# Kernel optimization log

Hardware: AMD Instinct MI355X
Metric: run time of the kernel (lower is better)

The kernel has to match this reference:

```python
import jax, jax.numpy as jnp
import numpy as np

N, C, L, K = 150000, 256, 50000, 200  # nodes, classes(=feature dim), labeled count, top-k


def setup_inputs() -> dict:
    key = jax.random.key(0)
    k1, k2 = jax.random.split(key)
    inputs = jax.random.normal(k1, (N, C), dtype=jnp.float32)
    cls = jax.random.randint(k2, (N,), 0, C)
    labels = jax.nn.one_hot(cls, C, dtype=jnp.float32)  # one-hot label matrix [N, C]
    labels_mask = jnp.arange(N) < L      # first L nodes labeled
    unlabels_mask = ~labels_mask
    return {"inputs": inputs, "labels": labels, "labels_mask": labels_mask,
            "unlabels_mask": unlabels_mask, "k": K}


def _l2n(x):
    # tf.nn.l2_normalize with epsilon 1e-12
    return x * jax.lax.rsqrt(jnp.maximum(jnp.sum(x * x, axis=-1, keepdims=True), 1e-12))


def reference(inputs, labels, labels_mask, unlabels_mask, k):
    lm = labels_mask.astype(inputs.dtype)    # [N]
    um = unlabels_mask.astype(inputs.dtype)  # [N]
    # protos: per-class mean of labeled features (masked matmul == boolean_mask + matmul)
    total = jnp.einsum('nf,nc->fc', inputs * lm[:, None], labels)  # [F, C]
    weight = 1.0 / jnp.sum(labels, 0)                               # 1/count per class (over ALL labels, as in TF)
    protos = (total * weight[None, :]).T                            # [C, F]
    # cosine similarity of every node to every prototype [N, C]
    prob = _l2n(inputs) @ _l2n(protos).T
    # per-row top-k, scattered back to a sparse [N, C] (raw top values, softmax in TF was dead code)
    vals, idx = jax.lax.top_k(prob, k)                              # [N, k]
    rows = jnp.arange(prob.shape[0])[:, None]
    sparse = jnp.zeros_like(prob).at[rows, idx].set(vals)
    p = sparse * um[:, None]                                        # only unlabeled rows contribute
    # per-class normalization: denom_c = sum_u p[u,c] + n_labeled_c
    denom = jnp.sum(p, 0) + jnp.sum(labels * lm[:, None], 0)        # [C]
    w = p / denom[None, :]                                          # [N, C]
    # change[c] = sum_u w[u,c] * (x_u - protos[c])
    change = w.T @ inputs - jnp.sum(w, 0)[:, None] * protos         # [C, F]
    protos = protos + change
    logits = _l2n(inputs) @ _l2n(protos).T                          # [N, C]
    return logits
```

## Files before the change

kernel.cpp:

```cpp
#include <hip/hip_runtime.h>

typedef unsigned int uint;
typedef unsigned short ushort;
typedef float f32x4 __attribute__((ext_vector_type(4)));
typedef uint u32x4 __attribute__((ext_vector_type(4)));
typedef uint u32x2 __attribute__((ext_vector_type(2)));
typedef __bf16 bf16x8 __attribute__((ext_vector_type(8)));

constexpr int NR = 150000;
constexpr int CD = 256;
constexpr int LR = 50000;
constexpr int KEX = 56;
constexpr int NB1 = 49984;
constexpr int NUP = 100032;
constexpr int NTP = 150080;
constexpr int NPB = NTP / 64;
constexpr int NCB = 1024;
constexpr int NFB = NPB + NCB;

__device__ __forceinline__ ushort f2bf(float x) {
  uint u = __builtin_bit_cast(uint, x);
  u += 0x7FFFu + ((u >> 16) & 1u);
  return (ushort)(u >> 16);
}
__device__ __forceinline__ uint key16(uint b) {
  return (b & 0x8000u) ? (~b & 0xFFFFu) : (b | 0x8000u);
}
__device__ __forceinline__ float bfval(uint p) {
  return __builtin_bit_cast(float, p << 16);
}

__global__ __launch_bounds__(256) void k_pre(const float* __restrict__ X,
                                             const float* __restrict__ labels,
                                             ushort* __restrict__ Xt,
                                             float* __restrict__ invn,
                                             int* __restrict__ cls,
                                             float* __restrict__ ca,
                                             float* __restrict__ cl) {
  __shared__ __align__(16) char sm[34816];
  int t = threadIdx.x;
  uint bx = blockIdx.x;
  uint ia = (bx * (uint)NCB) / (uint)NFB;
  uint ib = ((bx + 1) * (uint)NCB) / (uint)NFB;
  if (ib > ia) {
    int* ha = (int*)sm;
    int* hl = (int*)(sm + 1024);
    ha[t] = 0; hl[t] = 0;
    __syncthreads();
    int lane = t & 63;
    int wid = ((int)ia << 2) | (t >> 6);
    int nw = NCB << 2;
    int n = wid;
    for (; n + 3 * nw < NR; n += 4 * nw) {
      f32x4 v[4];
#pragma unroll
      for (int u = 0; u < 4; ++u)
        v[u] = *reinterpret_cast<const f32x4*>(&labels[(size_t)(n + u * nw) * CD + lane * 4]);
#pragma unroll
      for (int u = 0; u < 4; ++u) {
        int nn = n + u * nw;
        int j = v[u][0] > 0.5f ? 0 : v[u][1] > 0.5f ? 1 : v[u][2] > 0.5f ? 2
                                                        : v[u][3] > 0.5f ? 3 : -1;
        if (j >= 0) {
          int c = lane * 4 + j;
          cls[nn] = c;
          atomicAdd(&ha[c], 1);
          if (nn < LR) atomicAdd(&hl[c], 1);
        }
      }
    }
    for (; n < NR; n += nw) {
      f32x4 v = *reinterpret_cast<const f32x4*>(&labels[(size_t)n * CD + lane * 4]);
      int j = v[0] > 0.5f ? 0 : v[1] > 0.5f ? 1 : v[2] > 0.5f ? 2 : v[3] > 0.5f ? 3 : -1;
      if (j >= 0) {
        int c = lane * 4 + j;
        cls[n] = c;
        atomicAdd(&ha[c], 1);
        if (n < LR) atomicAdd(&hl[c], 1);
      }
    }
    __syncthreads();
    atomicAdd(&ca[t], (float)ha[t]);
    atomicAdd(&cl[t], (float)hl[t]);
  } else {
    int pb = (int)(bx - ia);
    ushort* xl = (ushort*)sm;
    float* red = (float*)(sm + 33792);
    int r = t >> 2, cq = t & 3;
    int g0 = pb * 64;
    int g = g0 + r;
    bool valid = g < NR;
    float ss = 0.f;
#pragma unroll
    for (int j = 0; j < 16; ++j) {
      int col = cq * 4 + j * 16;
      f32x4 x = valid ? *reinterpret_cast<const f32x4*>(&X[g * CD + col])
                      : (f32x4){0.f, 0.f, 0.f, 0.f};
      ss += x[0] * x[0] + x[1] * x[1] + x[2] * x[2] + x[3] * x[3];
      uint p0 = (uint)f2bf(x[0]) | ((uint)f2bf(x[1]) << 16);
      uint p1 = (uint)f2bf(x[2]) | ((uint)f2bf(x[3]) << 16);
      *reinterpret_cast<u32x2*>(&xl[r * 264 + col]) = (u32x2){p0, p1};
    }
    red[t] = ss;
    __syncthreads();
    if (t < 64) {
      float s4 = red[t * 4] + red[t * 4 + 1] + red[t * 4 + 2] + red[t * 4 + 3];
      if (g0 + t < NR) invn[g0 + t] = rsqrtf(fmaxf(s4, 1e-12f));
    }
    ushort* xp = Xt + (size_t)pb * 16384;
    int f = t;
    uint buf[4];
    for (int n = 0; n < 64; ++n) {
      ushort v16 = xl[n * 264 + f];
      int sl = n & 7;
      if (sl & 1) buf[sl >> 1] |= (uint)v16 << 16; else buf[sl >> 1] = v16;
      if (sl == 7)
        *reinterpret_cast<u32x4*>(&xp[f * 64 + n - 7]) =
            (u32x4){buf[0], buf[1], buf[2], buf[3]};
    }
  }
}

template <int KIND>
__global__ __launch_bounds__(1024) void k_gemmB(const int* __restrict__ cls,
                                                const ushort* __restrict__ Ap,
                                                const ushort* __restrict__ Xt,
                                                float* __restrict__ P,
                                                int nch, int nbase) {
  __shared__ __align__(16) ushort Al[256 * 40];
  __shared__ __align__(16) ushort Bl[256 * 40];
  int t = threadIdx.x;
  int lane = t & 63, w = t >> 6;
  int m = lane & 15, qd = lane >> 4;
  int cR = t >> 2, off = (t & 3) * 8;
  f32x4 acc[16];
#pragma unroll
  for (int i = 0; i < 16; ++i) acc[i] = (f32x4){0.f, 0.f, 0.f, 0.f};

  if (KIND == 0) {
    for (int i = t; i < 5120; i += 1024) reinterpret_cast<uint*>(Al)[i] = 0u;
  }

  u32x4 aR, bR;
  int curc = -1, prevc = -1;
  int ch = blockIdx.x;
  if (ch < nch) {
    int n0 = ch * 32;
    if (KIND == 1) {
      const ushort* ap = Ap + (size_t)(n0 >> 6) * 16384 + (n0 & 63);
      aR = *reinterpret_cast<const u32x4*>(&ap[cR * 64 + off]);
    } else if (t < 32) {
      int gg = n0 + t;
      curc = (gg < LR) ? cls[gg] : -1;
    }
    int gr = nbase + n0;
    const ushort* xp = Xt + (size_t)(gr >> 6) * 16384 + (gr & 63);
    bR = *reinterpret_cast<const u32x4*>(&xp[cR * 64 + off]);
  }

  for (; ch < nch; ch += gridDim.x) {
    __syncthreads();
    if (KIND == 0) {
      if (t < 32) {
        if (prevc >= 0) Al[prevc * 40 + t] = 0;
        if (curc >= 0) Al[curc * 40 + t] = 0x3F80;
        prevc = curc;
      }
    } else {
      *reinterpret_cast<u32x4*>(&Al[cR * 40 + off]) = aR;
    }
    *reinterpret_cast<u32x4*>(&Bl[cR * 40 + off]) = bR;
    int chn = ch + gridDim.x;
    if (chn < nch) {
      int n0 = chn * 32;
      if (KIND == 1) {
        const ushort* ap = Ap + (size_t)(n0 >> 6) * 16384 + (n0 & 63);
        aR = *reinterpret_cast<const u32x4*>(&ap[cR * 64 + off]);
      } else if (t < 32) {
        int gg = n0 + t;
        curc = (gg < LR) ? cls[gg] : -1;
      }
      int gr = nbase + n0;
      const ushort* xp = Xt + (size_t)(gr >> 6) * 16384 + (gr & 63);
      bR = *reinterpret_cast<const u32x4*>(&xp[cR * 64 + off]);
    }
    __syncthreads();
    bf16x8 a = *reinterpret_cast<const bf16x8*>(&Al[(w * 16 + m) * 40 + qd * 8]);
#pragma unroll
    for (int ft = 0; ft < 16; ++ft) {
      bf16x8 b = *reinterpret_cast<const bf16x8*>(&Bl[(ft * 16 + m) * 40 + qd * 8]);
      acc[ft] = __builtin_amdgcn_mfma_f32_16x16x32_bf16(a, b, acc[ft], 0, 0, 0);
    }
  }
  float* Ps = P + (size_t)blockIdx.x * 65536;
#pragma unroll
  for (int ft = 0; ft < 16; ++ft)
#pragma unroll
    for (int r = 0; r < 4; ++r)
      Ps[(w * 16 + qd * 4 + r) * 256 + ft * 16 + m] = acc[ft][r];
}

__global__ __launch_bounds__(256) void k_protos(const float* __restrict__ P, int nsl,
                                                const float* __restrict__ ca,
                                                float* __restrict__ protos,
                                                ushort* __restrict__ phat) {
  __shared__ float red[256];
  int c = blockIdx.x, f = threadIdx.x;
  float s = 0.f;
  for (int i = 0; i < nsl; ++i) s += P[i * 65536 + c * 256 + f];
  float cnt = ca[c];
  float pv = cnt > 0.5f ? s / cnt : 0.f;
  protos[c * 256 + f] = pv;
  red[f] = pv * pv;
  __syncthreads();
  for (int st = 128; st > 0; st >>= 1) {
    if (f < st) red[f] += red[f + st];
    __syncthreads();
  }
  float iv = rsqrtf(fmaxf(red[0], 1e-12f));
  phat[c * 256 + f] = f2bf(pv * iv);
}

__global__ __launch_bounds__(256) void k_update(const float* __restrict__ PS, int nsl,
                                                const float* __restrict__ protos,
                                                const float* __restrict__ q,
                                                const float* __restrict__ clab,
                                                ushort* __restrict__ phat2) {
  __shared__ float red[256];
  int c = blockIdx.x, f = threadIdx.x;
  float s = 0.f;
  for (int i = 0; i < nsl; ++i) s += PS[i * 65536 + c * 256 + f];
  float qc = q[c];
  float den = qc + clab[c];
  float pv = protos[c * 256 + f];
  float np = pv + (s - qc * pv) / den;
  red[f] = np * np;
  __syncthreads();
  for (int st = 128; st > 0; st >>= 1) {
    if (f < st) red[f] += red[f + st];
    __syncthreads();
  }
  float iv = rsqrtf(fmaxf(red[0], 1e-12f));
  phat2[c * 256 + f] = f2bf(np * iv);
}

template <int TOPK>
__global__ __launch_bounds__(256, 4) void k_passA(const float* __restrict__ X,
                                                  const float* __restrict__ invn,
                                                  const ushort* __restrict__ Bm,
                                                  float* __restrict__ out,
                                                  ushort* __restrict__ pt,
                                                  float* __restrict__ q,
                                                  int gbase) {
  __shared__ __align__(16) char smem[TOPK ? 35840 : 20480];
  ushort* Bl = reinterpret_cast<ushort*>(smem);
  float* qlds = reinterpret_cast<float*>(smem + 34816);
  int t = threadIdx.x;
  int lane = t & 63, w = t >> 6;
  int m = lane & 15, qd = lane >> 4;
  int g0 = gbase + blockIdx.x * 64;
  int g2 = g0 + w * 16 + m;
  bool vA = g2 < NR;
  float inv2 = vA ? invn[g2] : 0.f;
  const float* xp = X + (size_t)(vA ? g2 : 0) * CD + qd * 8;
  int cB = t >> 2, offB = (t & 3) * 8;
  if (TOPK) qlds[t] = 0.f;
  f32x4 acc[16];
#pragma unroll
  for (int i = 0; i < 16; ++i) acc[i] = (f32x4){0.f, 0.f, 0.f, 0.f};

  f32x4 x0 = *reinterpret_cast<const f32x4*>(&xp[0]);
  f32x4 x1 = *reinterpret_cast<const f32x4*>(&xp[4]);
  u32x4 bR[4];
#pragma unroll
  for (int i = 0; i < 4; ++i)
    bR[i] = *reinterpret_cast<const u32x4*>(&Bm[(cB + i * 64) * 256 + offB]);

  for (int k0 = 0; k0 < 256; k0 += 32) {
    f32x4 y0 = x0 * inv2, y1 = x1 * inv2;
    uint u0 = (uint)f2bf(y0[0]) | ((uint)f2bf(y0[1]) << 16);
    uint u1 = (uint)f2bf(y0[2]) | ((uint)f2bf(y0[3]) << 16);
    uint u2 = (uint)f2bf(y1[0]) | ((uint)f2bf(y1[1]) << 16);
    uint u3 = (uint)f2bf(y1[2]) | ((uint)f2bf(y1[3]) << 16);
    u32x4 au = (u32x4){u0, u1, u2, u3};
    bf16x8 a = __builtin_bit_cast(bf16x8, au);
    __syncthreads();
#pragma unroll
    for (int i = 0; i < 4; ++i)
      *reinterpret_cast<u32x4*>(&Bl[(cB + i * 64) * 40 + offB]) = bR[i];
    if (k0 < 224) {
      int kn = k0 + 32;
      x0 = *reinterpret_cast<const f32x4*>(&xp[kn]);
      x1 = *reinterpret_cast<const f32x4*>(&xp[kn + 4]);
#pragma unroll
      for (int i = 0; i < 4; ++i)
        bR[i] = *reinterpret_cast<const u32x4*>(
            &Bm[(cB + i * 64) * 256 + kn + offB]);
    }
    __syncthreads();
#pragma unroll
    for (int ft = 0; ft < 16; ++ft) {
      bf16x8 b = *reinterpret_cast<const bf16x8*>(&Bl[(ft * 16 + m) * 40 + qd * 8]);
      acc[ft] = __builtin_amdgcn_mfma_f32_16x16x32_bf16(a, b, acc[ft], 0, 0, 0);
    }
  }

  if constexpr (TOPK == 0) {
#pragma unroll
    for (int ft = 0; ft < 16; ++ft)
#pragma unroll
      for (int r = 0; r < 4; ++r) {
        int rr = w * 16 + qd * 4 + r;
        int gg = g0 + rr;
        if (gg < NR) out[gg * 256 + ft * 16 + m] = acc[ft][r];
      }
  } else {
    ushort* s16 = reinterpret_cast<ushort*>(smem);
    __syncthreads();
#pragma unroll
    for (int ft = 0; ft < 16; ++ft)
#pragma unroll
      for (int r = 0; r < 4; ++r)
        s16[(w * 16 + qd * 4 + r) * 272 + ft * 16 + m] = f2bf(acc[ft][r]);
    uint tk0 = 0, tk1 = 0, tk2 = 0, tk3 = 0;
    for (int i0 = 0; i0 < 16; i0 += 4) {
      uint kk[4][4];
      uint mth[4];
#pragma unroll
      for (int rr = 0; rr < 4; ++rr) {
        int rw = w * 16 + i0 + rr;
        u32x2 pk = *reinterpret_cast<const u32x2*>(&s16[rw * 272 + lane * 4]);
        kk[rr][0] = key16(pk[0] & 0xFFFFu);
        kk[rr][1] = key16(pk[0] >> 16);
        kk[rr][2] = key16(pk[1] & 0xFFFFu);
        kk[rr][3] = key16(pk[1] >> 16);
        mth[rr] = 0u;
      }
      for (int b = 15; b >= 0; --b) {
#pragma unroll
        for (int rr = 0; rr < 4; ++rr) {
          uint cand = mth[rr] | (1u << b);
          int cnt = __builtin_popcountll(__ballot(kk[rr][0] < cand)) +
                    __builtin_popcountll(__ballot(kk[rr][1] < cand)) +
                    __builtin_popcountll(__ballot(kk[rr][2] < cand)) +
                    __builtin_popcountll(__ballot(kk[rr][3] < cand));
          if (cnt <= KEX) mth[rr] = cand;
        }
      }
      if (i0 == (qd << 2)) { tk0 = mth[0]; tk1 = mth[1]; tk2 = mth[2]; tk3 = mth[3]; }
    }
    int brow = g0 + w * 16 + qd * 4;
    bool ok0 = (brow + 0 >= LR) && (brow + 0 < NR);
    bool ok1 = (brow + 1 >= LR) && (brow + 1 < NR);
    bool ok2 = (brow + 2 >= LR) && (brow + 2 < NR);
    bool ok3 = (brow + 3 >= LR) && (brow + 3 < NR);
    ushort* pp = pt + (size_t)blockIdx.x * 16384;
#pragma unroll
    for (int ft = 0; ft < 16; ++ft) {
      uint v0 = f2bf(acc[ft][0]), v1 = f2bf(acc[ft][1]);
      uint v2 = f2bf(acc[ft][2]), v3 = f2bf(acc[ft][3]);
      uint p0 = (ok0 && key16(v0) >= tk0) ? v0 : 0u;
      uint p1 = (ok1 && key16(v1) >= tk1) ? v1 : 0u;
      uint p2 = (ok2 && key16(v2) >= tk2) ? v2 : 0u;
      uint p3 = (ok3 && key16(v3) >= tk3) ? v3 : 0u;
      uint lo = p0 | (p1 << 16), hi = p2 | (p3 << 16);
      float qv = bfval(p0) + bfval(p1) + bfval(p2) + bfval(p3);
      uint plo = __shfl_xor(lo, 16);
      uint phi = __shfl_xor(hi, 16);
      if (qd & 1)
        *reinterpret_cast<u32x4*>(
            &pp[(ft * 16 + m) * 64 + w * 16 + (qd >> 1) * 8]) =
            (u32x4){plo, phi, lo, hi};
      atomicAdd(&qlds[ft * 16 + m], qv);
    }
    __syncthreads();
    atomicAdd(&q[t], qlds[t]);
  }
}

extern "C" void kernel_launch(void* const* d_in, const int* in_sizes, int n_in,
                              void* d_out, int out_size, void* d_ws, size_t ws_size,
                              hipStream_t stream) {
  const float* inputs = (const float*)d_in[0];
  const float* labels = (const float*)d_in[1];
  float* out = (float*)d_out;

  ushort* p_t = (ushort*)d_out;
  ushort* Xt  = (ushort*)((char*)d_out + (size_t)256 * NUP * 2);

  char* ws = (char*)d_ws;
  float* q      = (float*)(ws + 0);
  float* c_all  = (float*)(ws + 1024);
  float* c_lab  = (float*)(ws + 2048);
  float* protos = (float*)(ws + 4096);
  ushort* phat  = (ushort*)(ws + 4096 + 262144);
  ushort* phat2 = (ushort*)(ws + 4096 + 262144 + 131072);
  float* invn   = (float*)(ws + 528384);
  int*   cls    = (int*)(ws + 1128384);
  size_t base = 1736704;
  int sT = 256, sS = 256;
  while (base + (size_t)(sT + sS) * 262144ULL > ws_size) {
    if (sS > sT) sS >>= 1; else if (sT > 8) sT >>= 1; else break;
  }
  float* PT = (float*)(ws + base);
  float* PS = PT + (size_t)sT * 65536;

  hipMemsetAsync(ws, 0, 3072, stream);

  k_pre<<<NFB, 256, 0, stream>>>(inputs, labels, Xt, invn, cls, c_all, c_lab);
  k_gemmB<0><<<sT, 1024, 0, stream>>>(cls, nullptr, Xt, PT, 1563, 0);
  k_protos<<<256, 256, 0, stream>>>(PT, sT, c_all, protos, phat);
  k_passA<1><<<NUP / 64, 256, 0, stream>>>(inputs, invn, phat, nullptr, p_t, q, NB1);
  k_gemmB<1><<<sS, 1024, 0, stream>>>(nullptr, p_t, Xt, PS, NUP / 32, NB1);
  k_update<<<256, 256, 0, stream>>>(PS, sS, protos, q, c_lab, phat2);
  k_passA<0><<<(NR + 63) / 64, 256, 0, stream>>>(inputs, invn, phat2, out, nullptr, nullptr, 0);
}
```

Baseline: 717.9 us.

## Double K-step per sync in passA and halve preprocess block rows

The passA GEMM loop now stages 64 K-columns of prototypes per iteration instead of 32, which halves the number of barrier pairs and doubles the MFMA work between syncs. Occupancy drops from 4 to 3 blocks per CU to make room for the larger register and LDS footprint. The preprocessing kernel switches to 32-row transpose blocks with a fixed 2048 label-histogram blocks placed first, replacing the interleaved block-index mapping. An extra barrier and a moved qlds init are added around the top-k stage.

```diff
diff --git a/kernel.cpp b/kernel.cpp
--- a/kernel.cpp
+++ b/kernel.cpp
@@ -14,9 +14,9 @@
 constexpr int NB1 = 49984;
 constexpr int NUP = 100032;
 constexpr int NTP = 150080;
-constexpr int NPB = NTP / 64;
-constexpr int NCB = 1024;
-constexpr int NFB = NPB + NCB;
+constexpr int NPB = NTP / 32;
+constexpr int NCB = 2048;
+constexpr int NFB = NCB + NPB;
 
 __device__ __forceinline__ ushort f2bf(float x) {
   uint u = __builtin_bit_cast(uint, x);
@@ -37,18 +37,16 @@
                                              int* __restrict__ cls,
                                              float* __restrict__ ca,
                                              float* __restrict__ cl) {
-  __shared__ __align__(16) char sm[34816];
+  __shared__ __align__(16) char sm[17920];
   int t = threadIdx.x;
-  uint bx = blockIdx.x;
-  uint ia = (bx * (uint)NCB) / (uint)NFB;
-  uint ib = ((bx + 1) * (uint)NCB) / (uint)NFB;
-  if (ib > ia) {
+  int bx = blockIdx.x;
+  if (bx < NCB) {
     int* ha = (int*)sm;
     int* hl = (int*)(sm + 1024);
     ha[t] = 0; hl[t] = 0;
     __syncthreads();
     int lane = t & 63;
-    int wid = ((int)ia << 2) | (t >> 6);
+    int wid = (bx << 2) | (t >> 6);
     int nw = NCB << 2;
     int n = wid;
     for (; n + 3 * nw < NR; n += 4 * nw) {
@@ -83,18 +81,18 @@
     atomicAdd(&ca[t], (float)ha[t]);
     atomicAdd(&cl[t], (float)hl[t]);
   } else {
-    int pb = (int)(bx - ia);
+    int pb = bx - NCB;
     ushort* xl = (ushort*)sm;
-    float* red = (float*)(sm + 33792);
-    int r = t >> 2, cq = t & 3;
-    int g0 = pb * 64;
+    float* red = (float*)(sm + 16896);
+    int r = t >> 3, cq = t & 7;
+    int g0 = pb * 32;
     int g = g0 + r;
     bool valid = g < NR;
     float ss = 0.f;
 #pragma unroll
-    for (int j = 0; j < 16; ++j) {
-      int col = cq * 4 + j * 16;
-      f32x4 x = valid ? *reinterpret_cast<const f32x4*>(&X[g * CD + col])
+    for (int j = 0; j < 8; ++j) {
+      int col = cq * 4 + j * 32;
+      f32x4 x = valid ? *reinterpret_cast<const f32x4*>(&X[(size_t)g * CD + col])
                       : (f32x4){0.f, 0.f, 0.f, 0.f};
       ss += x[0] * x[0] + x[1] * x[1] + x[2] * x[2] + x[3] * x[3];
       uint p0 = (uint)f2bf(x[0]) | ((uint)f2bf(x[1]) << 16);
@@ -103,19 +101,21 @@
     }
     red[t] = ss;
     __syncthreads();
-    if (t < 64) {
-      float s4 = red[t * 4] + red[t * 4 + 1] + red[t * 4 + 2] + red[t * 4 + 3];
-      if (g0 + t < NR) invn[g0 + t] = rsqrtf(fmaxf(s4, 1e-12f));
-    }
-    ushort* xp = Xt + (size_t)pb * 16384;
+    if (t < 32) {
+      float s = red[t * 8] + red[t * 8 + 1] + red[t * 8 + 2] + red[t * 8 + 3] +
+                red[t * 8 + 4] + red[t * 8 + 5] + red[t * 8 + 6] + red[t * 8 + 7];
+      if (g0 + t < NR) invn[g0 + t] = rsqrtf(fmaxf(s, 1e-12f));
+    }
+    ushort* xp = Xt + (size_t)(pb >> 1) * 16384;
+    int hh = (pb & 1) * 32;
     int f = t;
     uint buf[4];
-    for (int n = 0; n < 64; ++n) {
+    for (int n = 0; n < 32; ++n) {
       ushort v16 = xl[n * 264 + f];
       int sl = n & 7;
       if (sl & 1) buf[sl >> 1] |= (uint)v16 << 16; else buf[sl >> 1] = v16;
       if (sl == 7)
-        *reinterpret_cast<u32x4*>(&xp[f * 64 + n - 7]) =
+        *reinterpret_cast<u32x4*>(&xp[f * 64 + hh + n - 7]) =
             (u32x4){buf[0], buf[1], buf[2], buf[3]};
     }
   }
@@ -245,16 +245,15 @@
 }
 
 template <int TOPK>
-__global__ __launch_bounds__(256, 4) void k_passA(const float* __restrict__ X,
+__global__ __launch_bounds__(256, 3) void k_passA(const float* __restrict__ X,
                                                   const float* __restrict__ invn,
                                                   const ushort* __restrict__ Bm,
                                                   float* __restrict__ out,
                                                   ushort* __restrict__ pt,
                                                   float* __restrict__ q,
                                                   int gbase) {
-  __shared__ __align__(16) char smem[TOPK ? 35840 : 20480];
+  __shared__ __align__(16) char smem[36864];
   ushort* Bl = reinterpret_cast<ushort*>(smem);
-  float* qlds = reinterpret_cast<float*>(smem + 34816);
   int t = threadIdx.x;
   int lane = t & 63, w = t >> 6;
   int m = lane & 15, qd = lane >> 4;
@@ -264,44 +263,62 @@
   float inv2 = vA ? invn[g2] : 0.f;
   const float* xp = X + (size_t)(vA ? g2 : 0) * CD + qd * 8;
   int cB = t >> 2, offB = (t & 3) * 8;
-  if (TOPK) qlds[t] = 0.f;
   f32x4 acc[16];
 #pragma unroll
   for (int i = 0; i < 16; ++i) acc[i] = (f32x4){0.f, 0.f, 0.f, 0.f};
 
   f32x4 x0 = *reinterpret_cast<const f32x4*>(&xp[0]);
   f32x4 x1 = *reinterpret_cast<const f32x4*>(&xp[4]);
-  u32x4 bR[4];
-#pragma unroll
-  for (int i = 0; i < 4; ++i)
-    bR[i] = *reinterpret_cast<const u32x4*>(&Bm[(cB + i * 64) * 256 + offB]);
-
-  for (int k0 = 0; k0 < 256; k0 += 32) {
-    f32x4 y0 = x0 * inv2, y1 = x1 * inv2;
-    uint u0 = (uint)f2bf(y0[0]) | ((uint)f2bf(y0[1]) << 16);
-    uint u1 = (uint)f2bf(y0[2]) | ((uint)f2bf(y0[3]) << 16);
-    uint u2 = (uint)f2bf(y1[0]) | ((uint)f2bf(y1[1]) << 16);
-    uint u3 = (uint)f2bf(y1[2]) | ((uint)f2bf(y1[3]) << 16);
-    u32x4 au = (u32x4){u0, u1, u2, u3};
-    bf16x8 a = __builtin_bit_cast(bf16x8, au);
-    __syncthreads();
-#pragma unroll
-    for (int i = 0; i < 4; ++i)
-      *reinterpret_cast<u32x4*>(&Bl[(cB + i * 64) * 40 + offB]) = bR[i];
-    if (k0 < 224) {
-      int kn = k0 + 32;
+  f32x4 x2 = *reinterpret_cast<const f32x4*>(&xp[32]);
+  f32x4 x3 = *reinterpret_cast<const f32x4*>(&xp[36]);
+  u32x4 bR[8];
+#pragma unroll
+  for (int i = 0; i < 4; ++i) {
+    bR[2 * i] = *reinterpret_cast<const u32x4*>(&Bm[(cB + i * 64) * 256 + offB]);
+    bR[2 * i + 1] =
+        *reinterpret_cast<const u32x4*>(&Bm[(cB + i * 64) * 256 + 32 + offB]);
+  }
+
+  for (int k0 = 0; k0 < 256; k0 += 64) {
+    f32x4 y0 = x0 * inv2, y1 = x1 * inv2, y2 = x2 * inv2, y3 = x3 * inv2;
+    u32x4 au0 = (u32x4){(uint)f2bf(y0[0]) | ((uint)f2bf(y0[1]) << 16),
+                        (uint)f2bf(y0[2]) | ((uint)f2bf(y0[3]) << 16),
+                        (uint)f2bf(y1[0]) | ((uint)f2bf(y1[1]) << 16),
+                        (uint)f2bf(y1[2]) | ((uint)f2bf(y1[3]) << 16)};
+    u32x4 au1 = (u32x4){(uint)f2bf(y2[0]) | ((uint)f2bf(y2[1]) << 16),
+                        (uint)f2bf(y2[2]) | ((uint)f2bf(y2[3]) << 16),
+                        (uint)f2bf(y3[0]) | ((uint)f2bf(y3[1]) << 16),
+                        (uint)f2bf(y3[2]) | ((uint)f2bf(y3[3]) << 16)};
+    bf16x8 a0 = __builtin_bit_cast(bf16x8, au0);
+    bf16x8 a1 = __builtin_bit_cast(bf16x8, au1);
+    __syncthreads();
+#pragma unroll
+    for (int i = 0; i < 4; ++i) {
+      *reinterpret_cast<u32x4*>(&Bl[(cB + i * 64) * 72 + offB]) = bR[2 * i];
+      *reinterpret_cast<u32x4*>(&Bl[(cB + i * 64) * 72 + 32 + offB]) = bR[2 * i + 1];
+    }
+    if (k0 < 192) {
+      int kn = k0 + 64;
       x0 = *reinterpret_cast<const f32x4*>(&xp[kn]);
       x1 = *reinterpret_cast<const f32x4*>(&xp[kn + 4]);
-#pragma unroll
-      for (int i = 0; i < 4; ++i)
-        bR[i] = *reinterpret_cast<const u32x4*>(
+      x2 = *reinterpret_cast<const f32x4*>(&xp[kn + 32]);
+      x3 = *reinterpret_cast<const f32x4*>(&xp[kn + 36]);
+#pragma unroll
+      for (int i = 0; i < 4; ++i) {
+        bR[2 * i] = *reinterpret_cast<const u32x4*>(
             &Bm[(cB + i * 64) * 256 + kn + offB]);
+        bR[2 * i + 1] = *reinterpret_cast<const u32x4*>(
+            &Bm[(cB + i * 64) * 256 + kn + 32 + offB]);
+      }
     }
     __syncthreads();
 #pragma unroll
     for (int ft = 0; ft < 16; ++ft) {
-      bf16x8 b = *reinterpret_cast<const bf16x8*>(&Bl[(ft * 16 + m) * 40 + qd * 8]);
-      acc[ft] = __builtin_amdgcn_mfma_f32_16x16x32_bf16(a, b, acc[ft], 0, 0, 0);
+      bf16x8 b0 = *reinterpret_cast<const bf16x8*>(&Bl[(ft * 16 + m) * 72 + qd * 8]);
+      acc[ft] = __builtin_amdgcn_mfma_f32_16x16x32_bf16(a0, b0, acc[ft], 0, 0, 0);
+      bf16x8 b1 =
+          *reinterpret_cast<const bf16x8*>(&Bl[(ft * 16 + m) * 72 + 32 + qd * 8]);
+      acc[ft] = __builtin_amdgcn_mfma_f32_16x16x32_bf16(a1, b1, acc[ft], 0, 0, 0);
     }
   }
 
@@ -316,7 +333,9 @@
       }
   } else {
     ushort* s16 = reinterpret_cast<ushort*>(smem);
-    __syncthreads();
+    float* qlds = reinterpret_cast<float*>(smem + 34816);
+    __syncthreads();
+    qlds[t] = 0.f;
 #pragma unroll
     for (int ft = 0; ft < 16; ++ft)
 #pragma unroll
@@ -349,6 +368,7 @@
       }
       if (i0 == (qd << 2)) { tk0 = mth[0]; tk1 = mth[1]; tk2 = mth[2]; tk3 = mth[3]; }
     }
+    __syncthreads();
     int brow = g0 + w * 16 + qd * 4;
     bool ok0 = (brow + 0 >= LR) && (brow + 0 < NR);
     bool ok1 = (brow + 1 >= LR) && (brow + 1 < NR);
```

New measurement: 760.7 us. 6.0% more time.
